# Optimization experiments

Measured on AMD Instinct MI355X. Metric: run time of the kernel, lower is better.

Reference implementation:

```python
import jax, jax.numpy as jnp
import numpy as np

NUM_HEADS = 8

def setup_inputs() -> dict:
    key0 = jax.random.key(0)
    ks = jax.random.split(key0, 6)
    T, S, B, E = 2048, 2048, 2, 256
    W_SCALE = 0.06  # ~xavier_uniform std for 256x256
    return {
        "query": jax.random.normal(ks[0], (T, B, E), dtype=jnp.float32),
        "key": jax.random.normal(ks[1], (S, B, E), dtype=jnp.float32),
        "value": jax.random.normal(ks[2], (S, B, E), dtype=jnp.float32),
        "Wq": jax.random.normal(ks[3], (E, E), dtype=jnp.float32) * W_SCALE,
        "bq": jnp.zeros((E,), dtype=jnp.float32),
        "Wk": jax.random.normal(ks[4], (E, E), dtype=jnp.float32) * W_SCALE,
        "bk": jnp.zeros((E,), dtype=jnp.float32),
        "Wo": jax.random.normal(ks[5], (E, E), dtype=jnp.float32) * W_SCALE,
        "bo": jnp.zeros((E,), dtype=jnp.float32),
    }

def reference(query, key, value, Wq, bq, Wk, bk, Wo, bo):
    # query: [T,B,E], key/value: [S,B,E]
    T, B, E = query.shape
    S = key.shape[0]
    H = NUM_HEADS
    Dh = E // H
    q = jnp.einsum('tbe,fe->tbf', query, Wq) + bq
    k = jnp.einsum('sbe,fe->sbf', key, Wk) + bk
    # split heads: view(L, B*H, Dh) == reshape(L, B, H, Dh)
    qh = q.reshape(T, B, H, Dh)
    kh = k.reshape(S, B, H, Dh)
    vh = value.reshape(S, B, H, Dh)  # v is NOT projected in this module
    scale = 1.0 / jnp.sqrt(jnp.asarray(Dh, dtype=query.dtype))
    scores = jnp.einsum('tbhd,sbhd->bhts', qh * scale, kh)  # [B,H,T,S]
    attn = jax.nn.softmax(scores, axis=-1)
    out = jnp.einsum('bhts,sbhd->tbhd', attn, vh).reshape(T, B, E)
    # residual output projection: out + linear(out)
    out = out + jnp.einsum('tbe,fe->tbf', out, Wo) + bo
    avg_weights = jnp.mean(attn, axis=1)  # [B,T,S]
    return (out, avg_weights)
```

## Files before the change

kernel.cpp:

```cpp
#include <hip/hip_runtime.h>
#include <hip/hip_fp16.h>

#define T_DIM 2048
#define S_DIM 2048
#define B_DIM 2
#define E_DIM 256
#define H_DIM 8
#define DH 32

typedef _Float16 half8 __attribute__((ext_vector_type(8)));
typedef _Float16 half4 __attribute__((ext_vector_type(4)));
typedef float floatx4 __attribute__((ext_vector_type(4)));

#if defined(__has_builtin)
#if __has_builtin(__builtin_amdgcn_exp2f)
#define EXPFN(x) __builtin_amdgcn_exp2f(x)
#define LOG2E_FOLD 1.4426950408889634f
#endif
#endif
#ifndef EXPFN
#define EXPFN(x) __expf(x)
#define LOG2E_FOLD 1.0f
#endif

__global__ __launch_bounds__(256) void prep_kernel(const float* __restrict__ V,
                                                   _Float16* __restrict__ Vt2,
                                                   const float* __restrict__ Wq,
                                                   const float* __restrict__ Wk,
                                                   const float* __restrict__ Wo,
                                                   _Float16* __restrict__ Wqh,
                                                   _Float16* __restrict__ Wkh,
                                                   _Float16* __restrict__ Woh) {
  __shared__ float tile[64][33];
  int tid = threadIdx.x;
  int bx = blockIdx.x;
  if (bx < 512) {
    int st = bx & 31, h = (bx >> 5) & 7, b = bx >> 8;
    int s0 = st * 64;
    int d = tid & 31, sr = tid >> 5;
#pragma unroll
    for (int k = 0; k < 8; ++k) {
      int s = sr + k * 8;
      tile[s][d] = V[((size_t)(s0 + s) * B_DIM + b) * E_DIM + h * DH + d];
    }
    __syncthreads();
    int si = tid & 63, dq = tid >> 6;
    size_t base = ((size_t)b * H_DIM + h) * 128 * 512;
    int tl = st * 4 + (si >> 4);
    int sl = si & 15;
#pragma unroll
    for (int m = 0; m < 8; ++m) {
      int dd = dq * 8 + m;
      Vt2[base + (size_t)tl * 512 + dd * 16 + sl] = (_Float16)tile[si][dd];
    }
  } else {
    int i = (bx - 512) * 2048 + tid * 8;
    int sel = i >> 16, off = i & 65535;
    const float* src = sel == 0 ? Wq : (sel == 1 ? Wk : Wo);
    _Float16* dst = sel == 0 ? Wqh : (sel == 1 ? Wkh : Woh);
    float4 a0 = *(const float4*)(src + off);
    float4 a1 = *(const float4*)(src + off + 4);
    half8 hv;
    hv[0]=(_Float16)a0.x; hv[1]=(_Float16)a0.y; hv[2]=(_Float16)a0.z; hv[3]=(_Float16)a0.w;
    hv[4]=(_Float16)a1.x; hv[5]=(_Float16)a1.y; hv[6]=(_Float16)a1.z; hv[7]=(_Float16)a1.w;
    if (sel == 2) {
      int f = off >> 8, e0 = off & 255;
      int di = f - e0;
      if (di >= 0 && di < 8) hv[di] += (_Float16)1.0f;
    }
    *(half8*)(dst + off) = hv;
  }
}

#define XS 264
__global__ __launch_bounds__(256, 4) void proj_mfma(const float* __restrict__ Q,
                                                    const float* __restrict__ K,
                                                    const _Float16* __restrict__ Wqh,
                                                    const _Float16* __restrict__ Wkh,
                                                    const float* __restrict__ bq,
                                                    const float* __restrict__ bk,
                                                    _Float16* __restrict__ Qp,
                                                    _Float16* __restrict__ Kp,
                                                    float scale_q) {
  __shared__ _Float16 Xs[64 * XS];
  int z = blockIdx.z;
  const float* X = z ? K : Q;
  const _Float16* Wh = z ? Wkh : Wqh;
  const float* bias = z ? bk : bq;
  _Float16* out = z ? Kp : Qp;
  float scale = z ? 1.0f : scale_q;

  int tid = threadIdx.x;
  int lane = tid & 63, w = tid >> 6;
  int quad = lane >> 4, l16 = lane & 15;
  int r0 = blockIdx.x * 64;
  int c0 = blockIdx.y * 64;

#pragma unroll
  for (int it = 0; it < 16; ++it) {
    int row = (tid >> 6) + it * 4, col = (tid & 63) * 4;
    float4 a = *(const float4*)(X + (size_t)(r0 + row) * 256 + col);
    half4 hv;
    hv[0] = (_Float16)a.x; hv[1] = (_Float16)a.y;
    hv[2] = (_Float16)a.z; hv[3] = (_Float16)a.w;
    *(half4*)(Xs + row * XS + col) = hv;
  }
  __syncthreads();

  floatx4 c[4] = {{0.f,0.f,0.f,0.f},{0.f,0.f,0.f,0.f},{0.f,0.f,0.f,0.f},{0.f,0.f,0.f,0.f}};
  int arow = w * 16 + l16;
#pragma unroll
  for (int k0 = 0; k0 < 256; k0 += 32) {
    half8 af = *(const half8*)(Xs + arow * XS + k0 + quad * 8);
#pragma unroll
    for (int j = 0; j < 4; ++j) {
      int f = c0 + j * 16 + l16;
      half8 bf = *(const half8*)(Wh + (size_t)f * 256 + k0 + quad * 8);
      c[j] = __builtin_amdgcn_mfma_f32_16x16x32_f16(af, bf, c[j], 0, 0, 0);
    }
  }
#pragma unroll
  for (int j = 0; j < 4; ++j) {
    int f = c0 + j * 16 + l16;
    float bv = bias[f];
    int h = f >> 5, d = f & 31;
#pragma unroll
    for (int r = 0; r < 4; ++r) {
      int row = r0 + w * 16 + quad * 4 + r;
      int t = row >> 1, b = row & 1;
      out[(((size_t)b * H_DIM + h) * T_DIM + t) * DH + d] =
          (_Float16)((c[j][r] + bv) * scale);
    }
  }
}

#define OSTRIDE 36
__global__ __launch_bounds__(512, 2) void attn_o_kernel(const _Float16* __restrict__ Qp,
                                                        const _Float16* __restrict__ Kp,
                                                        const _Float16* __restrict__ Vt2,
                                                        _Float16* __restrict__ Of16,
                                                        float* __restrict__ lsum) {
  __shared__ float stageO[8][64 * OSTRIDE];
  __shared__ float lstage[8][64];

  int tid = threadIdx.x;
  int lane = tid & 63, w = tid >> 6;
  int quad = lane >> 4, l16 = lane & 15;
  int bx = blockIdx.x;
  int h = bx & 7, b = (bx >> 3) & 1, tcc = bx >> 4;
  int t0 = tcc << 6;

  const _Float16* Qb = Qp + (((size_t)b * H_DIM + h) * T_DIM + t0) * DH;
  const _Float16* Kb = Kp + ((size_t)b * H_DIM + h) * S_DIM * DH;
  const _Float16* Vb = Vt2 + ((size_t)b * H_DIM + h) * 128 * 512;

  half8 qf[4];
#pragma unroll
  for (int j = 0; j < 4; ++j)
    qf[j] = *(const half8*)(Qb + (size_t)(j * 16 + l16) * DH + quad * 8);

  floatx4 o[4][2];
#pragma unroll
  for (int j = 0; j < 4; ++j) { o[j][0] = (floatx4){0,0,0,0}; o[j][1] = (floatx4){0,0,0,0}; }
  float ls[4] = {0.f, 0.f, 0.f, 0.f};

  int tile0 = w * 16;
  half8 kf[2];
  half4 v0[2], v1[2];
  kf[0] = *(const half8*)(Kb + (size_t)(tile0 * 16 + l16) * DH + quad * 8);
  v0[0] = *(const half4*)(Vb + (size_t)tile0 * 512 + l16 * 16 + quad * 4);
  v1[0] = *(const half4*)(Vb + (size_t)tile0 * 512 + 256 + l16 * 16 + quad * 4);

#pragma unroll
  for (int i = 0; i < 16; ++i) {
    int cur = i & 1, nxt = cur ^ 1;
    if (i < 15) {
      int tl = tile0 + i + 1;
      kf[nxt] = *(const half8*)(Kb + (size_t)(tl * 16 + l16) * DH + quad * 8);
      v0[nxt] = *(const half4*)(Vb + (size_t)tl * 512 + l16 * 16 + quad * 4);
      v1[nxt] = *(const half4*)(Vb + (size_t)tl * 512 + 256 + l16 * 16 + quad * 4);
    }
#pragma unroll
    for (int j = 0; j < 4; ++j) {
      floatx4 c = {0.f, 0.f, 0.f, 0.f};
      c = __builtin_amdgcn_mfma_f32_16x16x32_f16(kf[cur], qf[j], c, 0, 0, 0);
      float e0 = EXPFN(c[0]), e1 = EXPFN(c[1]), e2 = EXPFN(c[2]), e3 = EXPFN(c[3]);
      ls[j] += (e0 + e1) + (e2 + e3);
      half4 p;
      p[0] = (_Float16)e0; p[1] = (_Float16)e1; p[2] = (_Float16)e2; p[3] = (_Float16)e3;
      o[j][0] = __builtin_amdgcn_mfma_f32_16x16x16f16(p, v0[cur], o[j][0], 0, 0, 0);
      o[j][1] = __builtin_amdgcn_mfma_f32_16x16x16f16(p, v1[cur], o[j][1], 0, 0, 0);
    }
  }

#pragma unroll
  for (int j = 0; j < 4; ++j) {
    float v = ls[j];
    v += __shfl_xor(v, 16, 64);
    v += __shfl_xor(v, 32, 64);
    if (quad == 0) lstage[w][j * 16 + l16] = v;
  }
#pragma unroll
  for (int j = 0; j < 4; ++j)
#pragma unroll
    for (int r = 0; r < 4; ++r) {
      stageO[w][(j * 16 + quad * 4 + r) * OSTRIDE + l16] = o[j][0][r];
      stageO[w][(j * 16 + quad * 4 + r) * OSTRIDE + 16 + l16] = o[j][1][r];
    }
  __syncthreads();

  int t = tid >> 3, d0 = (tid & 7) * 4;
  floatx4 os = {0.f, 0.f, 0.f, 0.f};
  float lr = 0.f;
#pragma unroll
  for (int ww = 0; ww < 8; ++ww) {
    os += *(const floatx4*)&stageO[ww][t * OSTRIDE + d0];
    lr += lstage[ww][t];
  }
  float rl = 1.0f / lr;
  half4 oh;
  oh[0] = (_Float16)(os[0] * rl); oh[1] = (_Float16)(os[1] * rl);
  oh[2] = (_Float16)(os[2] * rl); oh[3] = (_Float16)(os[3] * rl);
  *(half4*)(Of16 + ((size_t)(t0 + t) * B_DIM + b) * E_DIM + h * DH + d0) = oh;
  if (tid < 64) {
    float s = 0.f;
#pragma unroll
    for (int ww = 0; ww < 8; ++ww) s += lstage[ww][tid];
    lsum[((size_t)b * H_DIM + h) * T_DIM + t0 + tid] = s;
  }
}

#define ASTRIDE 132
__global__ __launch_bounds__(512, 2) void avg_kernel(const _Float16* __restrict__ Qp,
                                                     const _Float16* __restrict__ Kp,
                                                     const float* __restrict__ lsum,
                                                     float* __restrict__ avg_out) {
  __shared__ float ldsA[128 * ASTRIDE];

  int tid = threadIdx.x;
  int lane = tid & 63, w = tid >> 6;
  int quad = lane >> 4, l16 = lane & 15;
  int bx = blockIdx.x;
  int sc = bx & 15, tc = (bx >> 4) & 15, b = bx >> 8;
  int t0 = tc * 128, s0 = sc * 128;
  int tw = t0 + w * 16;

  floatx4 acc[8];
#pragma unroll
  for (int st = 0; st < 8; ++st) acc[st] = (floatx4){0.f, 0.f, 0.f, 0.f};

  for (int h = 0; h < H_DIM; ++h) {
    const _Float16* Qb = Qp + (((size_t)b * H_DIM + h) * T_DIM + tw) * DH;
    const _Float16* Kb = Kp + (((size_t)b * H_DIM + h) * S_DIM + s0) * DH;
    half8 qfrag = *(const half8*)(Qb + (size_t)l16 * DH + quad * 8);
    float rlv = 0.125f / lsum[((size_t)b * H_DIM + h) * T_DIM + tw + l16];
#pragma unroll
    for (int st = 0; st < 8; ++st) {
      half8 kf = *(const half8*)(Kb + (size_t)(st * 16 + l16) * DH + quad * 8);
      floatx4 c = {0.f, 0.f, 0.f, 0.f};
      c = __builtin_amdgcn_mfma_f32_16x16x32_f16(kf, qfrag, c, 0, 0, 0);
#pragma unroll
      for (int r = 0; r < 4; ++r) acc[st][r] += EXPFN(c[r]) * rlv;
    }
  }
#pragma unroll
  for (int st = 0; st < 8; ++st)
    *(floatx4*)&ldsA[(w * 16 + l16) * ASTRIDE + st * 16 + quad * 4] = acc[st];
  __syncthreads();

  int rbase = tid >> 4, seg = tid & 15;
#pragma unroll
  for (int rr = 0; rr < 4; ++rr) {
    int row = rr * 32 + rbase;
    const float* srcl = &ldsA[row * ASTRIDE];
    float* dst = avg_out + ((size_t)b * T_DIM + t0 + row) * S_DIM + s0;
#pragma unroll
    for (int k = 0; k < 2; ++k) {
      int col = seg * 4 + k * 64;
      *(floatx4*)(dst + col) = *(const floatx4*)(srcl + col);
    }
  }
}

__global__ __launch_bounds__(256, 4) void outproj_mfma(const _Float16* __restrict__ Of16,
                                                       const _Float16* __restrict__ Woh,
                                                       const float* __restrict__ bo,
                                                       float* __restrict__ out) {
  __shared__ _Float16 Os[64 * XS];
  int tid = threadIdx.x;
  int lane = tid & 63, w = tid >> 6;
  int quad = lane >> 4, l16 = lane & 15;
  int r0 = blockIdx.x * 64;
  int c0 = blockIdx.y * 64;

#pragma unroll
  for (int it = 0; it < 8; ++it) {
    int row = (tid >> 5) + it * 8, col = (tid & 31) * 8;
    *(half8*)(Os + row * XS + col) =
        *(const half8*)(Of16 + (size_t)(r0 + row) * 256 + col);
  }
  __syncthreads();

  floatx4 c[4] = {{0.f,0.f,0.f,0.f},{0.f,0.f,0.f,0.f},{0.f,0.f,0.f,0.f},{0.f,0.f,0.f,0.f}};
  int arow = w * 16 + l16;
#pragma unroll
  for (int k0 = 0; k0 < 256; k0 += 32) {
    half8 af = *(const half8*)(Os + arow * XS + k0 + quad * 8);
#pragma unroll
    for (int j = 0; j < 4; ++j) {
      int f = c0 + j * 16 + l16;
      half8 bf = *(const half8*)(Woh + (size_t)f * 256 + k0 + quad * 8);
      c[j] = __builtin_amdgcn_mfma_f32_16x16x32_f16(af, bf, c[j], 0, 0, 0);
    }
  }
#pragma unroll
  for (int j = 0; j < 4; ++j) {
    int f = c0 + j * 16 + l16;
    float bv = bo[f];
#pragma unroll
    for (int r = 0; r < 4; ++r) {
      int row = r0 + w * 16 + quad * 4 + r;
      out[(size_t)row * 256 + f] = c[j][r] + bv;
    }
  }
}

extern "C" void kernel_launch(void* const* d_in, const int* in_sizes, int n_in,
                              void* d_out, int out_size, void* d_ws, size_t ws_size,
                              hipStream_t stream) {
  const float* query = (const float*)d_in[0];
  const float* key   = (const float*)d_in[1];
  const float* value = (const float*)d_in[2];
  const float* Wq    = (const float*)d_in[3];
  const float* bq    = (const float*)d_in[4];
  const float* Wk    = (const float*)d_in[5];
  const float* bk    = (const float*)d_in[6];
  const float* Wo    = (const float*)d_in[7];
  const float* bo    = (const float*)d_in[8];

  float* out = (float*)d_out;
  float* avg_out = out + (size_t)T_DIM * B_DIM * E_DIM;

  char* ws = (char*)d_ws;
  _Float16* Qp   = (_Float16*)ws;
  _Float16* Kp   = (_Float16*)(ws + (2u << 20));
  _Float16* Vt2  = (_Float16*)(ws + (4u << 20));
  _Float16* Of16 = (_Float16*)(ws + (6u << 20));
  float*    lsum = (float*)(ws + (8u << 20));
  _Float16* Wqh  = (_Float16*)(ws + (8u << 20) + (128u << 10));
  _Float16* Wkh  = (_Float16*)(ws + (8u << 20) + (256u << 10));
  _Float16* Woh  = (_Float16*)(ws + (8u << 20) + (384u << 10));

  const float scale_q = 0.17677669529663687f * LOG2E_FOLD;

  prep_kernel<<<dim3(608), dim3(256), 0, stream>>>(value, Vt2, Wq, Wk, Wo, Wqh, Wkh, Woh);
  proj_mfma<<<dim3(64, 4, 2), dim3(256), 0, stream>>>(query, key, Wqh, Wkh, bq, bk,
                                                      Qp, Kp, scale_q);
  attn_o_kernel<<<dim3(512), dim3(512), 0, stream>>>(Qp, Kp, Vt2, Of16, lsum);
  avg_kernel<<<dim3(512), dim3(512), 0, stream>>>(Qp, Kp, lsum, avg_out);
  outproj_mfma<<<dim3(64, 4), dim3(256), 0, stream>>>(Of16, Woh, bo, out);
}
```

Baseline: 139.7 us.

## Merge five launches into three by fusing projection, V transpose, avg and outproj

Folds the fp16 weight conversion into the Q/K projection blocks, which now stage W tiles in LDS. The V transpose runs as extra blocks of the same launch. The out-projection is merged into the avg_weights kernel as extra blocks that convert Wo, with its +I residual fold, on the fly, and two launch_bounds occupancy hints are raised to 4. This removes two kernel launches and their inter-kernel gaps, at the cost of redundant per-block weight conversion and larger LDS use per block.

```diff
diff --git a/kernel.cpp b/kernel.cpp
--- a/kernel.cpp
+++ b/kernel.cpp
@@ -23,19 +23,76 @@
 #define LOG2E_FOLD 1.0f
 #endif
 
-__global__ __launch_bounds__(256) void prep_kernel(const float* __restrict__ V,
-                                                   _Float16* __restrict__ Vt2,
-                                                   const float* __restrict__ Wq,
-                                                   const float* __restrict__ Wk,
-                                                   const float* __restrict__ Wo,
-                                                   _Float16* __restrict__ Wqh,
-                                                   _Float16* __restrict__ Wkh,
-                                                   _Float16* __restrict__ Woh) {
-  __shared__ float tile[64][33];
+#define XS 264
+
+__global__ __launch_bounds__(256, 4) void k1_proj_vt(
+    const float* __restrict__ Q, const float* __restrict__ K,
+    const float* __restrict__ V,
+    const float* __restrict__ Wq, const float* __restrict__ Wk,
+    const float* __restrict__ bq, const float* __restrict__ bk,
+    _Float16* __restrict__ Qp, _Float16* __restrict__ Kp,
+    _Float16* __restrict__ Vt2, float scale_q) {
+  __shared__ __align__(16) _Float16 smem[2 * 64 * XS];
   int tid = threadIdx.x;
   int bx = blockIdx.x;
   if (bx < 512) {
-    int st = bx & 31, h = (bx >> 5) & 7, b = bx >> 8;
+    int z = bx >> 8;
+    int rem = bx & 255;
+    int r0 = (rem >> 2) * 64;
+    int c0 = (rem & 3) * 64;
+    const float* X = z ? K : Q;
+    const float* W = z ? Wk : Wq;
+    const float* bias = z ? bk : bq;
+    _Float16* outp = z ? Kp : Qp;
+    float scale = z ? 1.0f : scale_q;
+    _Float16* Xs = smem;
+    _Float16* Ws = smem + 64 * XS;
+    int lane = tid & 63, w = tid >> 6;
+    int quad = lane >> 4, l16 = lane & 15;
+#pragma unroll
+    for (int it = 0; it < 16; ++it) {
+      int row = (tid >> 6) + it * 4, col = (tid & 63) * 4;
+      float4 a = *(const float4*)(X + (size_t)(r0 + row) * 256 + col);
+      half4 hx;
+      hx[0] = (_Float16)a.x; hx[1] = (_Float16)a.y;
+      hx[2] = (_Float16)a.z; hx[3] = (_Float16)a.w;
+      *(half4*)(Xs + row * XS + col) = hx;
+      float4 wv = *(const float4*)(W + (size_t)(c0 + row) * 256 + col);
+      half4 hw;
+      hw[0] = (_Float16)wv.x; hw[1] = (_Float16)wv.y;
+      hw[2] = (_Float16)wv.z; hw[3] = (_Float16)wv.w;
+      *(half4*)(Ws + row * XS + col) = hw;
+    }
+    __syncthreads();
+
+    floatx4 c[4] = {{0.f,0.f,0.f,0.f},{0.f,0.f,0.f,0.f},{0.f,0.f,0.f,0.f},{0.f,0.f,0.f,0.f}};
+    int arow = w * 16 + l16;
+#pragma unroll
+    for (int k0 = 0; k0 < 256; k0 += 32) {
+      half8 af = *(const half8*)(Xs + arow * XS + k0 + quad * 8);
+#pragma unroll
+      for (int j = 0; j < 4; ++j) {
+        half8 bf = *(const half8*)(Ws + (j * 16 + l16) * XS + k0 + quad * 8);
+        c[j] = __builtin_amdgcn_mfma_f32_16x16x32_f16(af, bf, c[j], 0, 0, 0);
+      }
+    }
+#pragma unroll
+    for (int j = 0; j < 4; ++j) {
+      int f = c0 + j * 16 + l16;
+      float bv = bias[f];
+      int h = f >> 5, d = f & 31;
+#pragma unroll
+      for (int r = 0; r < 4; ++r) {
+        int row = r0 + w * 16 + quad * 4 + r;
+        int t = row >> 1, b = row & 1;
+        outp[(((size_t)b * H_DIM + h) * T_DIM + t) * DH + d] =
+            (_Float16)((c[j][r] + bv) * scale);
+      }
+    }
+  } else {
+    float (*tile)[33] = (float (*)[33])smem;
+    int b2 = bx - 512;
+    int st = b2 & 31, h = (b2 >> 5) & 7, b = b2 >> 8;
     int s0 = st * 64;
     int d = tid & 31, sr = tid >> 5;
 #pragma unroll
@@ -53,89 +110,11 @@
       int dd = dq * 8 + m;
       Vt2[base + (size_t)tl * 512 + dd * 16 + sl] = (_Float16)tile[si][dd];
     }
-  } else {
-    int i = (bx - 512) * 2048 + tid * 8;
-    int sel = i >> 16, off = i & 65535;
-    const float* src = sel == 0 ? Wq : (sel == 1 ? Wk : Wo);
-    _Float16* dst = sel == 0 ? Wqh : (sel == 1 ? Wkh : Woh);
-    float4 a0 = *(const float4*)(src + off);
-    float4 a1 = *(const float4*)(src + off + 4);
-    half8 hv;
-    hv[0]=(_Float16)a0.x; hv[1]=(_Float16)a0.y; hv[2]=(_Float16)a0.z; hv[3]=(_Float16)a0.w;
-    hv[4]=(_Float16)a1.x; hv[5]=(_Float16)a1.y; hv[6]=(_Float16)a1.z; hv[7]=(_Float16)a1.w;
-    if (sel == 2) {
-      int f = off >> 8, e0 = off & 255;
-      int di = f - e0;
-      if (di >= 0 && di < 8) hv[di] += (_Float16)1.0f;
-    }
-    *(half8*)(dst + off) = hv;
   }
 }
 
-#define XS 264
-__global__ __launch_bounds__(256, 4) void proj_mfma(const float* __restrict__ Q,
-                                                    const float* __restrict__ K,
-                                                    const _Float16* __restrict__ Wqh,
-                                                    const _Float16* __restrict__ Wkh,
-                                                    const float* __restrict__ bq,
-                                                    const float* __restrict__ bk,
-                                                    _Float16* __restrict__ Qp,
-                                                    _Float16* __restrict__ Kp,
-                                                    float scale_q) {
-  __shared__ _Float16 Xs[64 * XS];
-  int z = blockIdx.z;
-  const float* X = z ? K : Q;
-  const _Float16* Wh = z ? Wkh : Wqh;
-  const float* bias = z ? bk : bq;
-  _Float16* out = z ? Kp : Qp;
-  float scale = z ? 1.0f : scale_q;
-
-  int tid = threadIdx.x;
-  int lane = tid & 63, w = tid >> 6;
-  int quad = lane >> 4, l16 = lane & 15;
-  int r0 = blockIdx.x * 64;
-  int c0 = blockIdx.y * 64;
-
-#pragma unroll
-  for (int it = 0; it < 16; ++it) {
-    int row = (tid >> 6) + it * 4, col = (tid & 63) * 4;
-    float4 a = *(const float4*)(X + (size_t)(r0 + row) * 256 + col);
-    half4 hv;
-    hv[0] = (_Float16)a.x; hv[1] = (_Float16)a.y;
-    hv[2] = (_Float16)a.z; hv[3] = (_Float16)a.w;
-    *(half4*)(Xs + row * XS + col) = hv;
-  }
-  __syncthreads();
-
-  floatx4 c[4] = {{0.f,0.f,0.f,0.f},{0.f,0.f,0.f,0.f},{0.f,0.f,0.f,0.f},{0.f,0.f,0.f,0.f}};
-  int arow = w * 16 + l16;
-#pragma unroll
-  for (int k0 = 0; k0 < 256; k0 += 32) {
-    half8 af = *(const half8*)(Xs + arow * XS + k0 + quad * 8);
-#pragma unroll
-    for (int j = 0; j < 4; ++j) {
-      int f = c0 + j * 16 + l16;
-      half8 bf = *(const half8*)(Wh + (size_t)f * 256 + k0 + quad * 8);
-      c[j] = __builtin_amdgcn_mfma_f32_16x16x32_f16(af, bf, c[j], 0, 0, 0);
-    }
-  }
-#pragma unroll
-  for (int j = 0; j < 4; ++j) {
-    int f = c0 + j * 16 + l16;
-    float bv = bias[f];
-    int h = f >> 5, d = f & 31;
-#pragma unroll
-    for (int r = 0; r < 4; ++r) {
-      int row = r0 + w * 16 + quad * 4 + r;
-      int t = row >> 1, b = row & 1;
-      out[(((size_t)b * H_DIM + h) * T_DIM + t) * DH + d] =
-          (_Float16)((c[j][r] + bv) * scale);
-    }
-  }
-}
-
 #define OSTRIDE 36
-__global__ __launch_bounds__(512, 2) void attn_o_kernel(const _Float16* __restrict__ Qp,
+__global__ __launch_bounds__(512, 4) void attn_o_kernel(const _Float16* __restrict__ Qp,
                                                         const _Float16* __restrict__ Kp,
                                                         const _Float16* __restrict__ Vt2,
                                                         _Float16* __restrict__ Of16,
@@ -231,96 +210,96 @@
 }
 
 #define ASTRIDE 132
-__global__ __launch_bounds__(512, 2) void avg_kernel(const _Float16* __restrict__ Qp,
-                                                     const _Float16* __restrict__ Kp,
-                                                     const float* __restrict__ lsum,
-                                                     float* __restrict__ avg_out) {
-  __shared__ float ldsA[128 * ASTRIDE];
-
+__global__ __launch_bounds__(512, 4) void k3_avg_outproj(
+    const _Float16* __restrict__ Qp, const _Float16* __restrict__ Kp,
+    const float* __restrict__ lsum, const _Float16* __restrict__ Of16,
+    const float* __restrict__ Wo, const float* __restrict__ bo,
+    float* __restrict__ avg_out, float* __restrict__ out) {
+  __shared__ __align__(16) float smem[128 * ASTRIDE];
   int tid = threadIdx.x;
   int lane = tid & 63, w = tid >> 6;
   int quad = lane >> 4, l16 = lane & 15;
   int bx = blockIdx.x;
-  int sc = bx & 15, tc = (bx >> 4) & 15, b = bx >> 8;
-  int t0 = tc * 128, s0 = sc * 128;
-  int tw = t0 + w * 16;
-
-  floatx4 acc[8];
-#pragma unroll
-  for (int st = 0; st < 8; ++st) acc[st] = (floatx4){0.f, 0.f, 0.f, 0.f};
-
-  for (int h = 0; h < H_DIM; ++h) {
-    const _Float16* Qb = Qp + (((size_t)b * H_DIM + h) * T_DIM + tw) * DH;
-    const _Float16* Kb = Kp + (((size_t)b * H_DIM + h) * S_DIM + s0) * DH;
-    half8 qfrag = *(const half8*)(Qb + (size_t)l16 * DH + quad * 8);
-    float rlv = 0.125f / lsum[((size_t)b * H_DIM + h) * T_DIM + tw + l16];
-#pragma unroll
-    for (int st = 0; st < 8; ++st) {
-      half8 kf = *(const half8*)(Kb + (size_t)(st * 16 + l16) * DH + quad * 8);
-      floatx4 c = {0.f, 0.f, 0.f, 0.f};
-      c = __builtin_amdgcn_mfma_f32_16x16x32_f16(kf, qfrag, c, 0, 0, 0);
-#pragma unroll
-      for (int r = 0; r < 4; ++r) acc[st][r] += EXPFN(c[r]) * rlv;
-    }
-  }
-#pragma unroll
-  for (int st = 0; st < 8; ++st)
-    *(floatx4*)&ldsA[(w * 16 + l16) * ASTRIDE + st * 16 + quad * 4] = acc[st];
-  __syncthreads();
-
-  int rbase = tid >> 4, seg = tid & 15;
-#pragma unroll
-  for (int rr = 0; rr < 4; ++rr) {
-    int row = rr * 32 + rbase;
-    const float* srcl = &ldsA[row * ASTRIDE];
-    float* dst = avg_out + ((size_t)b * T_DIM + t0 + row) * S_DIM + s0;
-#pragma unroll
-    for (int k = 0; k < 2; ++k) {
-      int col = seg * 4 + k * 64;
-      *(floatx4*)(dst + col) = *(const floatx4*)(srcl + col);
-    }
-  }
-}
-
-__global__ __launch_bounds__(256, 4) void outproj_mfma(const _Float16* __restrict__ Of16,
-                                                       const _Float16* __restrict__ Woh,
-                                                       const float* __restrict__ bo,
-                                                       float* __restrict__ out) {
-  __shared__ _Float16 Os[64 * XS];
-  int tid = threadIdx.x;
-  int lane = tid & 63, w = tid >> 6;
-  int quad = lane >> 4, l16 = lane & 15;
-  int r0 = blockIdx.x * 64;
-  int c0 = blockIdx.y * 64;
-
-#pragma unroll
-  for (int it = 0; it < 8; ++it) {
-    int row = (tid >> 5) + it * 8, col = (tid & 31) * 8;
-    *(half8*)(Os + row * XS + col) =
-        *(const half8*)(Of16 + (size_t)(r0 + row) * 256 + col);
-  }
-  __syncthreads();
-
-  floatx4 c[4] = {{0.f,0.f,0.f,0.f},{0.f,0.f,0.f,0.f},{0.f,0.f,0.f,0.f},{0.f,0.f,0.f,0.f}};
-  int arow = w * 16 + l16;
-#pragma unroll
-  for (int k0 = 0; k0 < 256; k0 += 32) {
-    half8 af = *(const half8*)(Os + arow * XS + k0 + quad * 8);
+
+  if (bx < 512) {
+    int sc = bx & 15, tc = (bx >> 4) & 15, b = bx >> 8;
+    int t0 = tc * 128, s0 = sc * 128;
+    int tw = t0 + w * 16;
+
+    floatx4 acc[8];
+#pragma unroll
+    for (int st = 0; st < 8; ++st) acc[st] = (floatx4){0.f, 0.f, 0.f, 0.f};
+
+    for (int h = 0; h < H_DIM; ++h) {
+      const _Float16* Qb = Qp + (((size_t)b * H_DIM + h) * T_DIM + tw) * DH;
+      const _Float16* Kb = Kp + (((size_t)b * H_DIM + h) * S_DIM + s0) * DH;
+      half8 qfrag = *(const half8*)(Qb + (size_t)l16 * DH + quad * 8);
+      float rlv = 0.125f / lsum[((size_t)b * H_DIM + h) * T_DIM + tw + l16];
+#pragma unroll
+      for (int st = 0; st < 8; ++st) {
+        half8 kf = *(const half8*)(Kb + (size_t)(st * 16 + l16) * DH + quad * 8);
+        floatx4 c = {0.f, 0.f, 0.f, 0.f};
+        c = __builtin_amdgcn_mfma_f32_16x16x32_f16(kf, qfrag, c, 0, 0, 0);
+#pragma unroll
+        for (int r = 0; r < 4; ++r) acc[st][r] += EXPFN(c[r]) * rlv;
+      }
+    }
+#pragma unroll
+    for (int st = 0; st < 8; ++st)
+      *(floatx4*)&smem[(w * 16 + l16) * ASTRIDE + st * 16 + quad * 4] = acc[st];
+    __syncthreads();
+
+    int rbase = tid >> 4, seg = tid & 15;
+#pragma unroll
+    for (int rr = 0; rr < 4; ++rr) {
+      int row = rr * 32 + rbase;
+      const float* srcl = &smem[row * ASTRIDE];
+      float* dst = avg_out + ((size_t)b * T_DIM + t0 + row) * S_DIM + s0;
+#pragma unroll
+      for (int k = 0; k < 2; ++k) {
+        int col = seg * 4 + k * 64;
+        *(floatx4*)(dst + col) = *(const floatx4*)(srcl + col);
+      }
+    }
+  } else {
+    int bo_ = bx - 512;
+    int r0 = (bo_ >> 2) * 128;
+    int c0 = (bo_ & 3) * 64;
+    _Float16* Ws = (_Float16*)smem;
+#pragma unroll
+    for (int it = 0; it < 8; ++it) {
+      int row = (tid >> 6) + it * 8, col = (tid & 63) * 4;
+      int f = c0 + row;
+      float4 a = *(const float4*)(Wo + (size_t)f * 256 + col);
+      half4 hv;
+      hv[0] = (_Float16)a.x; hv[1] = (_Float16)a.y;
+      hv[2] = (_Float16)a.z; hv[3] = (_Float16)a.w;
+      int di = f - col;
+      if (di >= 0 && di < 4) hv[di] += (_Float16)1.0f;
+      *(half4*)(Ws + row * XS + col) = hv;
+    }
+    __syncthreads();
+
+    floatx4 c[4] = {{0.f,0.f,0.f,0.f},{0.f,0.f,0.f,0.f},{0.f,0.f,0.f,0.f},{0.f,0.f,0.f,0.f}};
+    int grow = r0 + w * 16 + l16;
+#pragma unroll
+    for (int k0 = 0; k0 < 256; k0 += 32) {
+      half8 af = *(const half8*)(Of16 + (size_t)grow * 256 + k0 + quad * 8);
+#pragma unroll
+      for (int j = 0; j < 4; ++j) {
+        half8 bf = *(const half8*)(Ws + (j * 16 + l16) * XS + k0 + quad * 8);
+        c[j] = __builtin_amdgcn_mfma_f32_16x16x32_f16(af, bf, c[j], 0, 0, 0);
+      }
+    }
 #pragma unroll
     for (int j = 0; j < 4; ++j) {
       int f = c0 + j * 16 + l16;
-      half8 bf = *(const half8*)(Woh + (size_t)f * 256 + k0 + quad * 8);
-      c[j] = __builtin_amdgcn_mfma_f32_16x16x32_f16(af, bf, c[j], 0, 0, 0);
-    }
-  }
-#pragma unroll
-  for (int j = 0; j < 4; ++j) {
-    int f = c0 + j * 16 + l16;
-    float bv = bo[f];
-#pragma unroll
-    for (int r = 0; r < 4; ++r) {
-      int row = r0 + w * 16 + quad * 4 + r;
-      out[(size_t)row * 256 + f] = c[j][r] + bv;
+      float bv = bo[f];
+#pragma unroll
+      for (int r = 0; r < 4; ++r) {
+        int row = r0 + w * 16 + quad * 4 + r;
+        out[(size_t)row * 256 + f] = c[j][r] + bv;
+      }
     }
   }
 }
@@ -347,16 +326,12 @@
   _Float16* Vt2  = (_Float16*)(ws + (4u << 20));
   _Float16* Of16 = (_Float16*)(ws + (6u << 20));
   float*    lsum = (float*)(ws + (8u << 20));
-  _Float16* Wqh  = (_Float16*)(ws + (8u << 20) + (128u << 10));
-  _Float16* Wkh  = (_Float16*)(ws + (8u << 20) + (256u << 10));
-  _Float16* Woh  = (_Float16*)(ws + (8u << 20) + (384u << 10));
 
   const float scale_q = 0.17677669529663687f * LOG2E_FOLD;
 
-  prep_kernel<<<dim3(608), dim3(256), 0, stream>>>(value, Vt2, Wq, Wk, Wo, Wqh, Wkh, Woh);
-  proj_mfma<<<dim3(64, 4, 2), dim3(256), 0, stream>>>(query, key, Wqh, Wkh, bq, bk,
-                                                      Qp, Kp, scale_q);
+  k1_proj_vt<<<dim3(1024), dim3(256), 0, stream>>>(query, key, value, Wq, Wk,
+                                                   bq, bk, Qp, Kp, Vt2, scale_q);
   attn_o_kernel<<<dim3(512), dim3(512), 0, stream>>>(Qp, Kp, Vt2, Of16, lsum);
-  avg_kernel<<<dim3(512), dim3(512), 0, stream>>>(Qp, Kp, lsum, avg_out);
-  outproj_mfma<<<dim3(64, 4), dim3(256), 0, stream>>>(Of16, Woh, bo, out);
+  k3_avg_outproj<<<dim3(640), dim3(512), 0, stream>>>(Qp, Kp, lsum, Of16, Wo, bo,
+                                                      avg_out, out);
 }
```

New measurement: 160.7 us. 1.15x slower.
